# Optimization experiments

Measured on AMD Instinct MI355X. Metric: run time of the kernel, lower is better.

The kernel has to match this reference:

```python
import jax, jax.numpy as jnp
import numpy as np

K = 1024          # num_embeddings
D = 256           # embedding_dim
COMMIT = 0.25
DECAY = 0.99
EPS = 1e-05


def setup_inputs() -> dict:
    key = jax.random.key(0)
    k1, k2 = jax.random.split(key)
    inputs = jax.random.normal(k1, (16, 4096, D), dtype=jnp.float32)
    weight = jax.random.normal(k2, (K, D), dtype=jnp.float32) * 0.1
    ema_cluster_size = jnp.zeros((K,), dtype=jnp.float32)
    ema_embedding_avg = weight  # initialized as a clone of the weights
    return {
        "inputs": inputs,
        "weight": weight,
        "ema_cluster_size": ema_cluster_size,
        "ema_embedding_avg": ema_embedding_avg,
    }


def reference(inputs, weight, ema_cluster_size, ema_embedding_avg):
    B = inputs.shape[0]
    flat = inputs.reshape(-1, D)                      # [N, D]
    dist = (
        jnp.sum(flat * flat, axis=1, keepdims=True)
        + jnp.sum(weight * weight, axis=1)
        - 2.0 * (flat @ weight.T)
    )                                                 # [N, K]
    idx = jnp.argmin(dist, axis=1)                    # [N] int
    # one-hot @ weight == gather
    quantized = weight[idx].reshape(inputs.shape)

    # --- EMA codebook update (training-mode side effects, returned as outputs) ---
    counts = jax.ops.segment_sum(jnp.ones_like(idx, dtype=jnp.float32), idx, num_segments=K)
    emb_sum = jax.ops.segment_sum(flat, idx, num_segments=K)  # one_hot.T @ flat
    new_cluster_size = DECAY * ema_cluster_size + (1.0 - DECAY) * counts
    new_embedding_avg = DECAY * ema_embedding_avg + (1.0 - DECAY) * emb_sum
    n = jnp.sum(new_cluster_size)
    cs = (new_cluster_size + EPS) / (n + K * EPS) * n
    new_weight = new_embedding_avg / cs[:, None]

    # --- losses + straight-through estimator ---
    e_latent_loss = jnp.mean((jax.lax.stop_gradient(quantized) - inputs) ** 2)
    q_latent_loss = jnp.mean((quantized - jax.lax.stop_gradient(inputs)) ** 2)
    vq_loss = q_latent_loss + COMMIT * e_latent_loss
    quantized_st = inputs + jax.lax.stop_gradient(quantized - inputs)

    return (
        quantized_st,
        vq_loss,
        idx.reshape(B, -1),
        new_weight,
        new_cluster_size,
        new_embedding_avg,
    )
```

## Files before the change

kernel.cpp:

```cpp
#include <hip/hip_runtime.h>

#define KC 1024
#define DD 256
#define NROWS 65536
#define BM 128
#define NT 512
#define RESCUE_EPS 0.02f
#define RB 8

typedef _Float16 f16x8 __attribute__((ext_vector_type(8)));
typedef __fp16 fp16x2 __attribute__((ext_vector_type(2)));
typedef float f32x4 __attribute__((ext_vector_type(4)));
typedef const __attribute__((address_space(1))) unsigned int* gptr_t;
typedef __attribute__((address_space(3))) unsigned int* lptr_t;

__global__ void wprep(const float* __restrict__ W, _Float16* __restrict__ wh,
                      float* __restrict__ se, float4* __restrict__ WT4) {
    int k = blockIdx.x, lane = threadIdx.x;
    float4 v = reinterpret_cast<const float4*>(W + (size_t)k * DD)[lane];
    union { fp16x2 h2[2]; uint2 u; } cv;
    cv.h2[0] = __builtin_amdgcn_cvt_pkrtz(v.x, v.y);
    cv.h2[1] = __builtin_amdgcn_cvt_pkrtz(v.z, v.w);
    *reinterpret_cast<uint2*>(wh + (size_t)k * DD + lane * 4) = cv.u;
    WT4[(size_t)lane * KC + k] = v;
    double s = (double)v.x * v.x + (double)v.y * v.y + (double)v.z * v.z + (double)v.w * v.w;
    for (int m = 32; m >= 1; m >>= 1) s += __shfl_xor(s, m, 64);
    if (lane == 0) se[k] = (float)s;
}

__global__ __launch_bounds__(NT, 2) void vq_mfma(
    const float* __restrict__ X,
    const _Float16* __restrict__ wh,
    const float* __restrict__ se,
    float* __restrict__ out_q, float* __restrict__ out_idx,
    int* __restrict__ idx_int, float* __restrict__ sx_out,
    int* __restrict__ flags, int* __restrict__ count,
    float* __restrict__ counts, double* __restrict__ loss_acc)
{
    __shared__ __align__(16) _Float16 wt[2][64 * 256];
    __shared__ float sxs[BM];
    __shared__ float ses[KC];
    __shared__ int argidx[BM];
    __shared__ double lred[8];

    const int tid = threadIdx.x;
    const int row0 = blockIdx.x * BM;
    const int w = tid >> 6, lane = tid & 63;
    const int m = lane & 15, g = lane >> 4;

    for (int i = tid; i < KC; i += NT) ses[i] = se[i];

    f16x8 ahr[8];
    {
        const float* xr = X + (size_t)(row0 + w * 16 + m) * DD;
        float p0 = 0.f, p1 = 0.f, p2 = 0.f, p3 = 0.f;
#pragma unroll
        for (int ks = 0; ks < 8; ++ks) {
            float4 a = *reinterpret_cast<const float4*>(xr + ks * 32 + g * 8);
            float4 b = *reinterpret_cast<const float4*>(xr + ks * 32 + g * 8 + 4);
            union { fp16x2 h2[4]; f16x8 h8; } cv;
            cv.h2[0] = __builtin_amdgcn_cvt_pkrtz(a.x, a.y);
            cv.h2[1] = __builtin_amdgcn_cvt_pkrtz(a.z, a.w);
            cv.h2[2] = __builtin_amdgcn_cvt_pkrtz(b.x, b.y);
            cv.h2[3] = __builtin_amdgcn_cvt_pkrtz(b.z, b.w);
            ahr[ks] = cv.h8;
            p0 = fmaf(a.x, a.x, fmaf(b.x, b.x, p0));
            p1 = fmaf(a.y, a.y, fmaf(b.y, b.y, p1));
            p2 = fmaf(a.z, a.z, fmaf(b.z, b.z, p2));
            p3 = fmaf(a.w, a.w, fmaf(b.w, b.w, p3));
        }
        float ss = (p0 + p1) + (p2 + p3);
        ss += __shfl_xor(ss, 16, 64);
        ss += __shfl_xor(ss, 32, 64);
        if (g == 0) sxs[w * 16 + m] = ss;
    }

    size_t srcoff[4];
    unsigned ldsoff[4];
#pragma unroll
    for (int p = 0; p < 4; ++p) {
        int gi = p * NT + tid;
        int code = gi >> 5, j = gi & 31;
        int kq = j ^ (code & 31);
        srcoff[p] = (size_t)code * DD + kq * 8;
        ldsoff[p] = gi * 8;
    }
    auto stage = [&](int ct, int buf) {
        const _Float16* b = wh + (size_t)ct * 64 * DD;
#pragma unroll
        for (int p = 0; p < 4; ++p)
            __builtin_amdgcn_global_load_lds((gptr_t)(const void*)(b + srcoff[p]),
                                             (lptr_t)(void*)&wt[buf][ldsoff[p]], 16, 0, 0);
    };

    stage(0, 0);
    __syncthreads();

    float b1[4], b2[4];
    int i1[4];
#pragma unroll
    for (int j = 0; j < 4; ++j) { b1[j] = 3.4e38f; b2[j] = 3.4e38f; i1[j] = 0; }

    float sxr[4];
#pragma unroll
    for (int j = 0; j < 4; ++j) sxr[j] = sxs[w * 16 + g * 4 + j];

    for (int ct = 0; ct < 16; ++ct) {
        const int buf = ct & 1;
        if (ct < 15) stage(ct + 1, buf ^ 1);

        const _Float16* wtb = wt[buf];
        f32x4 acc[4];
#pragma unroll
        for (int cs = 0; cs < 4; ++cs) acc[cs] = (f32x4){0.f, 0.f, 0.f, 0.f};

#pragma unroll
        for (int ks = 0; ks < 8; ++ks) {
            const int kq = ks * 4 + g;
#pragma unroll
            for (int cs = 0; cs < 4; ++cs) {
                const int code = cs * 16 + m;
                const int L = code * 32 + (kq ^ (code & 31));
                f16x8 bh = *reinterpret_cast<const f16x8*>(wtb + L * 8);
                acc[cs] = __builtin_amdgcn_mfma_f32_16x16x32_f16(ahr[ks], bh, acc[cs], 0, 0, 0);
            }
        }
#pragma unroll
        for (int cs = 0; cs < 4; ++cs) {
            const int code = ct * 64 + cs * 16 + m;
            const float sec = ses[code];
#pragma unroll
            for (int j = 0; j < 4; ++j) {
                float s = fmaf(-2.0f, acc[cs][j], sxr[j] + sec);
                if (s < b1[j]) { b2[j] = b1[j]; b1[j] = s; i1[j] = code; }
                else if (s < b2[j]) { b2[j] = s; }
            }
        }
        __syncthreads();
    }

#pragma unroll
    for (int j = 0; j < 4; ++j) {
        float v1 = b1[j], v2 = b2[j];
        int ix = i1[j];
        for (int mm = 1; mm < 16; mm <<= 1) {
            float ov1 = __shfl_xor(v1, mm, 64);
            int oi = __shfl_xor(ix, mm, 64);
            float ov2 = __shfl_xor(v2, mm, 64);
            float nv2 = fminf(fminf(v2, ov2), fmaxf(v1, ov1));
            if (ov1 < v1 || (ov1 == v1 && oi < ix)) { v1 = ov1; ix = oi; }
            v2 = nv2;
        }
        if (m == 0) {
            int rl = w * 16 + g * 4 + j;
            argidx[rl] = ix;
            if (v2 - v1 < RESCUE_EPS) {
                int p = atomicAdd(count, 1);
                flags[p] = row0 + rl;
            }
        }
    }
    __syncthreads();

    if (tid < BM) {
        int row = row0 + tid;
        int k = argidx[tid];
        idx_int[row] = k;
        out_idx[row] = (float)k;
        sx_out[row] = sxs[tid];
        atomicAdd(&counts[k], 1.0f);
    }

    {
        float lacc = 0.0f;
        const int rl = w * 16 + m;
        const int row = row0 + rl;
        const int k = argidx[rl];
        const _Float16* qh = wh + (size_t)k * DD;
        float* orow = out_q + (size_t)row * DD;
#pragma unroll
        for (int ks = 0; ks < 8; ++ks) {
            const int col = ks * 32 + g * 8;
            union { uint4 u; _Float16 h[8]; } qv, xv;
            qv.u = *reinterpret_cast<const uint4*>(qh + col);
            xv.u = *reinterpret_cast<uint4*>(&ahr[ks]);
            float o8[8];
#pragma unroll
            for (int q = 0; q < 8; ++q) {
                float qf = (float)qv.h[q];
                float df = qf - (float)xv.h[q];
                o8[q] = qf;
                lacc = fmaf(df, df, lacc);
            }
            *reinterpret_cast<float4*>(orow + col)     = *reinterpret_cast<float4*>(&o8[0]);
            *reinterpret_cast<float4*>(orow + col + 4) = *reinterpret_cast<float4*>(&o8[4]);
        }
        for (int mm = 32; mm >= 1; mm >>= 1) lacc += __shfl_xor(lacc, mm, 64);
        if (lane == 0) lred[w] = (double)lacc;
    }
    __syncthreads();
    if (tid == 0) {
        double t = 0.0;
        for (int i = 0; i < 8; ++i) t += lred[i];
        atomicAdd(loss_acc, t);
    }
}

__global__ __launch_bounds__(256) void rescue(
    const float* __restrict__ X, const float4* __restrict__ WT4,
    const float* __restrict__ Wf,
    const float* __restrict__ se, const float* __restrict__ sx,
    const int* __restrict__ flags, const int* __restrict__ count,
    int* __restrict__ idx_int, float* __restrict__ out_idx,
    float* __restrict__ out_q, float* __restrict__ counts,
    double* __restrict__ loss_acc)
{
    __shared__ __align__(16) float xs[RB][DD];
    __shared__ float rv[RB][256];
    __shared__ int ri[RB][256];
    __shared__ float sxr_s[RB];
    __shared__ int rows_s[RB];
    __shared__ int kn_s[RB], ko_s[RB];
    __shared__ double dred[4];
    const int t = threadIdx.x;
    const int n = count[0];

    for (int base = blockIdx.x * RB; base < n; base += gridDim.x * RB) {
        const int nb = min(RB, n - base);
        for (int idx = t; idx < nb * 64; idx += 256) {
            int r = idx >> 6, c4 = idx & 63;
            float4 v = reinterpret_cast<const float4*>(X + (size_t)flags[base + r] * DD)[c4];
            *reinterpret_cast<float4*>(&xs[r][c4 * 4]) = v;
        }
        if (t < nb) { rows_s[t] = flags[base + t]; sxr_s[t] = sx[flags[base + t]]; }
        __syncthreads();

        float acc[4][RB];
#pragma unroll
        for (int cc = 0; cc < 4; ++cc)
#pragma unroll
            for (int r = 0; r < RB; ++r) acc[cc][r] = 0.0f;

        float4 wv[4], wn[4];
#pragma unroll
        for (int cc = 0; cc < 4; ++cc) wv[cc] = WT4[(size_t)0 * KC + cc * 256 + t];

        for (int d4 = 0; d4 < 64; ++d4) {
            const int dn = (d4 < 63) ? d4 + 1 : 63;
#pragma unroll
            for (int cc = 0; cc < 4; ++cc) wn[cc] = WT4[(size_t)dn * KC + cc * 256 + t];
#pragma unroll
            for (int r = 0; r < RB; ++r) {
                float4 xv = *reinterpret_cast<const float4*>(&xs[r][d4 * 4]);
#pragma unroll
                for (int cc = 0; cc < 4; ++cc)
                    acc[cc][r] = fmaf(xv.w, wv[cc].w, fmaf(xv.z, wv[cc].z,
                                 fmaf(xv.y, wv[cc].y, fmaf(xv.x, wv[cc].x, acc[cc][r]))));
            }
#pragma unroll
            for (int cc = 0; cc < 4; ++cc) wv[cc] = wn[cc];
        }

        float best[RB];
        int bidx[RB];
#pragma unroll
        for (int r = 0; r < RB; ++r) { best[r] = 3.4e38f; bidx[r] = 0; }
#pragma unroll
        for (int cc = 0; cc < 4; ++cc) {
            const int c = cc * 256 + t;
            const float sec = se[c];
#pragma unroll
            for (int r = 0; r < RB; ++r) {
                float s = __fsub_rn(__fadd_rn(sxr_s[r], sec), __fmul_rn(2.0f, acc[cc][r]));
                if (s < best[r] || (s == best[r] && c < bidx[r])) { best[r] = s; bidx[r] = c; }
            }
        }
#pragma unroll
        for (int r = 0; r < RB; ++r) { rv[r][t] = best[r]; ri[r][t] = bidx[r]; }
        __syncthreads();

        for (int sft = 128; sft >= 1; sft >>= 1) {
            if (t < sft) {
#pragma unroll
                for (int r = 0; r < RB; ++r) {
                    float ov = rv[r][t + sft];
                    int oi = ri[r][t + sft];
                    if (ov < rv[r][t] || (ov == rv[r][t] && oi < ri[r][t])) {
                        rv[r][t] = ov; ri[r][t] = oi;
                    }
                }
            }
            __syncthreads();
        }
        if (t < nb) {
            int row = rows_s[t];
            int kn = ri[t][0], ko = idx_int[row];
            kn_s[t] = kn; ko_s[t] = ko;
            if (kn != ko) {
                idx_int[row] = kn;
                out_idx[row] = (float)kn;
                atomicAdd(&counts[ko], -1.0f);
                atomicAdd(&counts[kn], 1.0f);
            }
        }
        __syncthreads();

        for (int r = 0; r < nb; ++r) {
            const int ko = ko_s[r], kn = kn_s[r];
            if (kn != ko) {
                const int row = rows_s[r];
                float x = xs[r][t];
                float qo = Wf[(size_t)ko * DD + t];
                float qn = Wf[(size_t)kn * DD + t];
                float dfn = qn - x, dfo = qo - x;
                out_q[(size_t)row * DD + t] = x + dfn;
                double dl = (double)dfn * dfn - (double)dfo * dfo;
                for (int mm = 32; mm >= 1; mm >>= 1) dl += __shfl_xor(dl, mm, 64);
                if ((t & 63) == 0) dred[t >> 6] = dl;
                __syncthreads();
                if (t == 0) atomicAdd(loss_acc, dred[0] + dred[1] + dred[2] + dred[3]);
                __syncthreads();
            }
        }
        __syncthreads();
    }
}

__global__ void finprefix(const float* __restrict__ ema_cs, float* __restrict__ ncs_buf,
                          const double* __restrict__ loss_acc, float* __restrict__ out_loss,
                          float* __restrict__ n_out, int* __restrict__ off,
                          int* __restrict__ cur)
{
    __shared__ float red[1024];
    __shared__ int s[1024];
    int t = threadIdx.x;
    const float OM = (float)(1.0 - 0.99);
    float cnt = ncs_buf[t];
    s[t] = (int)cnt;
    float ncs = __fadd_rn(__fmul_rn(0.99f, ema_cs[t]), __fmul_rn(OM, cnt));
    ncs_buf[t] = ncs;
    red[t] = ncs;
    __syncthreads();
    for (int st = 512; st >= 1; st >>= 1) {
        if (t < st) red[t] += red[t + st];
        __syncthreads();
    }
    if (t == 0) {
        n_out[0] = red[0];
        float el = (float)(loss_acc[0] / 16777216.0);
        out_loss[0] = __fadd_rn(el, __fmul_rn(0.25f, el));
    }
    for (int d = 1; d < 1024; d <<= 1) {
        int v = (t >= d) ? s[t - d] : 0;
        __syncthreads();
        s[t] += v;
        __syncthreads();
    }
    off[t] = (t == 0) ? 0 : s[t - 1];
    cur[t] = 0;
    if (t == 0) off[1024] = NROWS;
}

__global__ __launch_bounds__(256) void scatter_rows(
    const int* __restrict__ idx_int, const int* __restrict__ off,
    int* __restrict__ cur, int* __restrict__ sorted) {
    int i = blockIdx.x * 256 + threadIdx.x;
    int k = idx_int[i];
    int p = atomicAdd(&cur[k], 1);
    sorted[off[k] + p] = i;
}

__global__ __launch_bounds__(256) void embfin2(
    const float* __restrict__ X, const int* __restrict__ off,
    const int* __restrict__ sorted, const float* __restrict__ ema_avg,
    const float* __restrict__ ncs, const float* __restrict__ n_ptr,
    float* __restrict__ out_avg, float* __restrict__ out_w)
{
    const int k = blockIdx.x, t = threadIdx.x;
    const int s0 = off[k], s1 = off[k + 1];
    float a0 = 0.f, a1 = 0.f, a2 = 0.f, a3 = 0.f;
    int i = s0;
    for (; i + 4 <= s1; i += 4) {
        int r0 = sorted[i], r1 = sorted[i + 1], r2 = sorted[i + 2], r3 = sorted[i + 3];
        a0 += X[(size_t)r0 * DD + t];
        a1 += X[(size_t)r1 * DD + t];
        a2 += X[(size_t)r2 * DD + t];
        a3 += X[(size_t)r3 * DD + t];
    }
    for (; i < s1; ++i) a0 += X[(size_t)sorted[i] * DD + t];
    float total = (a0 + a1) + (a2 + a3);

    const float OM = (float)(1.0 - 0.99);
    const float KEPS = (float)(1024.0 * 1e-5);
    size_t o = (size_t)k * DD + t;
    float avg = __fadd_rn(__fmul_rn(0.99f, ema_avg[o]), __fmul_rn(OM, total));
    float n = n_ptr[0];
    float cs = __fmul_rn(__fdiv_rn(__fadd_rn(ncs[k], 1e-5f), __fadd_rn(n, KEPS)), n);
    out_avg[o] = avg;
    out_w[o] = __fdiv_rn(avg, cs);
}

extern "C" void kernel_launch(void* const* d_in, const int* in_sizes, int n_in,
                              void* d_out, int out_size, void* d_ws, size_t ws_size,
                              hipStream_t stream) {
    const float* X = (const float*)d_in[0];
    const float* W = (const float*)d_in[1];
    const float* ema_cs = (const float*)d_in[2];
    const float* ema_avg = (const float*)d_in[3];

    float* out = (float*)d_out;
    float* out_q    = out;
    float* out_loss = out + 16777216;
    float* out_idx  = out + 16777217;
    float* out_w    = out + 16842753;
    float* out_ncs  = out + 17104897;
    float* out_avg  = out + 17105921;

    char* ws = (char*)d_ws;
    float* se      = (float*)(ws + 0);
    float* n_ptr   = (float*)(ws + 4096);
    double* loss   = (double*)(ws + 4112);
    int*   count   = (int*)(ws + 4128);
    _Float16* wh   = (_Float16*)(ws + 8192);
    float* sx      = (float*)(ws + 1056768);
    int*   idx_int = (int*)(ws + 1318912);
    int*   flags   = (int*)(ws + 1581056);
    float4* WT4    = (float4*)(ws + 2097152);
    int*   off     = (int*)(ws + 3145728);
    int*   cur     = (int*)(ws + 3153920);
    int*   sorted  = (int*)(ws + 3158016);

    hipMemsetAsync(out_ncs, 0, 1024 * sizeof(float), stream);
    hipMemsetAsync(loss, 0, sizeof(double), stream);
    hipMemsetAsync(count, 0, sizeof(int), stream);

    wprep<<<KC, 64, 0, stream>>>(W, wh, se, WT4);
    vq_mfma<<<NROWS / BM, NT, 0, stream>>>(X, wh, se, out_q, out_idx,
                                           idx_int, sx, flags, count,
                                           out_ncs, loss);
    rescue<<<512, 256, 0, stream>>>(X, WT4, W, se, sx, flags, count, idx_int, out_idx,
                                    out_q, out_ncs, loss);
    finprefix<<<1, 1024, 0, stream>>>(ema_cs, out_ncs, loss, out_loss, n_ptr, off, cur);
    scatter_rows<<<NROWS / 256, 256, 0, stream>>>(idx_int, off, cur, sorted);
    embfin2<<<KC, 256, 0, stream>>>(X, off, sorted, ema_avg, out_ncs, n_ptr,
                                    out_avg, out_w);
}
```

Measured before the change: 183.7 us.

## Give each wave two row tiles so codebook fragments are reused; fold memsets into wprep

The MFMA distance kernel now runs 256 threads per block, and each wave computes two 16-row tiles against every codebook fragment it reads from LDS. This halves the LDS reads per MFMA and raises the register footprint per thread. Staging now issues 8 global-to-LDS loads per thread to keep filling the same 64-code tile. The three hipMemsetAsync calls are removed and the zeroing of counts, loss and flag counter is done inside wprep, saving launch overhead.

New measurement: 175.8 us. 1.04x faster.

```diff
diff --git a/kernel.cpp b/kernel.cpp
--- a/kernel.cpp
+++ b/kernel.cpp
@@ -4,7 +4,7 @@
 #define DD 256
 #define NROWS 65536
 #define BM 128
-#define NT 512
+#define NT 256
 #define RESCUE_EPS 0.02f
 #define RB 8
 
@@ -15,7 +15,9 @@
 typedef __attribute__((address_space(3))) unsigned int* lptr_t;
 
 __global__ void wprep(const float* __restrict__ W, _Float16* __restrict__ wh,
-                      float* __restrict__ se, float4* __restrict__ WT4) {
+                      float* __restrict__ se, float4* __restrict__ WT4,
+                      float* __restrict__ counts, double* __restrict__ loss,
+                      int* __restrict__ flagcnt) {
     int k = blockIdx.x, lane = threadIdx.x;
     float4 v = reinterpret_cast<const float4*>(W + (size_t)k * DD)[lane];
     union { fp16x2 h2[2]; uint2 u; } cv;
@@ -25,7 +27,11 @@
     WT4[(size_t)lane * KC + k] = v;
     double s = (double)v.x * v.x + (double)v.y * v.y + (double)v.z * v.z + (double)v.w * v.w;
     for (int m = 32; m >= 1; m >>= 1) s += __shfl_xor(s, m, 64);
-    if (lane == 0) se[k] = (float)s;
+    if (lane == 0) {
+        se[k] = (float)s;
+        counts[k] = 0.0f;
+        if (k == 0) { loss[0] = 0.0; flagcnt[0] = 0; }
+    }
 }
 
 __global__ __launch_bounds__(NT, 2) void vq_mfma(
@@ -41,7 +47,7 @@
     __shared__ float sxs[BM];
     __shared__ float ses[KC];
     __shared__ int argidx[BM];
-    __shared__ double lred[8];
+    __shared__ double lred[4];
 
     const int tid = threadIdx.x;
     const int row0 = blockIdx.x * BM;
@@ -50,9 +56,10 @@
 
     for (int i = tid; i < KC; i += NT) ses[i] = se[i];
 
-    f16x8 ahr[8];
-    {
-        const float* xr = X + (size_t)(row0 + w * 16 + m) * DD;
+    f16x8 ahr[2][8];
+#pragma unroll
+    for (int rt = 0; rt < 2; ++rt) {
+        const float* xr = X + (size_t)(row0 + w * 32 + rt * 16 + m) * DD;
         float p0 = 0.f, p1 = 0.f, p2 = 0.f, p3 = 0.f;
 #pragma unroll
         for (int ks = 0; ks < 8; ++ks) {
@@ -63,7 +70,7 @@
             cv.h2[1] = __builtin_amdgcn_cvt_pkrtz(a.z, a.w);
             cv.h2[2] = __builtin_amdgcn_cvt_pkrtz(b.x, b.y);
             cv.h2[3] = __builtin_amdgcn_cvt_pkrtz(b.z, b.w);
-            ahr[ks] = cv.h8;
+            ahr[rt][ks] = cv.h8;
             p0 = fmaf(a.x, a.x, fmaf(b.x, b.x, p0));
             p1 = fmaf(a.y, a.y, fmaf(b.y, b.y, p1));
             p2 = fmaf(a.z, a.z, fmaf(b.z, b.z, p2));
@@ -72,23 +79,22 @@
         float ss = (p0 + p1) + (p2 + p3);
         ss += __shfl_xor(ss, 16, 64);
         ss += __shfl_xor(ss, 32, 64);
-        if (g == 0) sxs[w * 16 + m] = ss;
-    }
-
-    size_t srcoff[4];
-    unsigned ldsoff[4];
-#pragma unroll
-    for (int p = 0; p < 4; ++p) {
+        if (g == 0) sxs[w * 32 + rt * 16 + m] = ss;
+    }
+
+    unsigned srcoff[8], ldsoff[8];
+#pragma unroll
+    for (int p = 0; p < 8; ++p) {
         int gi = p * NT + tid;
         int code = gi >> 5, j = gi & 31;
         int kq = j ^ (code & 31);
-        srcoff[p] = (size_t)code * DD + kq * 8;
+        srcoff[p] = (unsigned)(code * DD + kq * 8);
         ldsoff[p] = gi * 8;
     }
     auto stage = [&](int ct, int buf) {
         const _Float16* b = wh + (size_t)ct * 64 * DD;
 #pragma unroll
-        for (int p = 0; p < 4; ++p)
+        for (int p = 0; p < 8; ++p)
             __builtin_amdgcn_global_load_lds((gptr_t)(const void*)(b + srcoff[p]),
                                              (lptr_t)(void*)&wt[buf][ldsoff[p]], 16, 0, 0);
     };
@@ -96,23 +102,30 @@
     stage(0, 0);
     __syncthreads();
 
-    float b1[4], b2[4];
-    int i1[4];
-#pragma unroll
-    for (int j = 0; j < 4; ++j) { b1[j] = 3.4e38f; b2[j] = 3.4e38f; i1[j] = 0; }
-
-    float sxr[4];
-#pragma unroll
-    for (int j = 0; j < 4; ++j) sxr[j] = sxs[w * 16 + g * 4 + j];
+    float b1[2][4], b2[2][4];
+    int i1[2][4];
+#pragma unroll
+    for (int rt = 0; rt < 2; ++rt)
+#pragma unroll
+        for (int j = 0; j < 4; ++j) { b1[rt][j] = 3.4e38f; b2[rt][j] = 3.4e38f; i1[rt][j] = 0; }
+
+    float sxr[2][4];
+#pragma unroll
+    for (int rt = 0; rt < 2; ++rt)
+#pragma unroll
+        for (int j = 0; j < 4; ++j) sxr[rt][j] = sxs[w * 32 + rt * 16 + g * 4 + j];
 
     for (int ct = 0; ct < 16; ++ct) {
         const int buf = ct & 1;
         if (ct < 15) stage(ct + 1, buf ^ 1);
 
         const _Float16* wtb = wt[buf];
-        f32x4 acc[4];
-#pragma unroll
-        for (int cs = 0; cs < 4; ++cs) acc[cs] = (f32x4){0.f, 0.f, 0.f, 0.f};
+        f32x4 acc0[4], acc1[4];
+#pragma unroll
+        for (int cs = 0; cs < 4; ++cs) {
+            acc0[cs] = (f32x4){0.f, 0.f, 0.f, 0.f};
+            acc1[cs] = (f32x4){0.f, 0.f, 0.f, 0.f};
+        }
 
 #pragma unroll
         for (int ks = 0; ks < 8; ++ks) {
@@ -122,7 +135,8 @@
                 const int code = cs * 16 + m;
                 const int L = code * 32 + (kq ^ (code & 31));
                 f16x8 bh = *reinterpret_cast<const f16x8*>(wtb + L * 8);
-                acc[cs] = __builtin_amdgcn_mfma_f32_16x16x32_f16(ahr[ks], bh, acc[cs], 0, 0, 0);
+                acc0[cs] = __builtin_amdgcn_mfma_f32_16x16x32_f16(ahr[0][ks], bh, acc0[cs], 0, 0, 0);
+                acc1[cs] = __builtin_amdgcn_mfma_f32_16x16x32_f16(ahr[1][ks], bh, acc1[cs], 0, 0, 0);
             }
         }
 #pragma unroll
@@ -130,36 +144,42 @@
             const int code = ct * 64 + cs * 16 + m;
             const float sec = ses[code];
 #pragma unroll
-            for (int j = 0; j < 4; ++j) {
-                float s = fmaf(-2.0f, acc[cs][j], sxr[j] + sec);
-                if (s < b1[j]) { b2[j] = b1[j]; b1[j] = s; i1[j] = code; }
-                else if (s < b2[j]) { b2[j] = s; }
-            }
-        }
-        __syncthreads();
-    }
-
-#pragma unroll
-    for (int j = 0; j < 4; ++j) {
-        float v1 = b1[j], v2 = b2[j];
-        int ix = i1[j];
-        for (int mm = 1; mm < 16; mm <<= 1) {
-            float ov1 = __shfl_xor(v1, mm, 64);
-            int oi = __shfl_xor(ix, mm, 64);
-            float ov2 = __shfl_xor(v2, mm, 64);
-            float nv2 = fminf(fminf(v2, ov2), fmaxf(v1, ov1));
-            if (ov1 < v1 || (ov1 == v1 && oi < ix)) { v1 = ov1; ix = oi; }
-            v2 = nv2;
-        }
-        if (m == 0) {
-            int rl = w * 16 + g * 4 + j;
-            argidx[rl] = ix;
-            if (v2 - v1 < RESCUE_EPS) {
-                int p = atomicAdd(count, 1);
-                flags[p] = row0 + rl;
-            }
-        }
-    }
+            for (int rt = 0; rt < 2; ++rt) {
+                f32x4 A = rt ? acc1[cs] : acc0[cs];
+#pragma unroll
+                for (int j = 0; j < 4; ++j) {
+                    float s = fmaf(-2.0f, A[j], sxr[rt][j] + sec);
+                    if (s < b1[rt][j]) { b2[rt][j] = b1[rt][j]; b1[rt][j] = s; i1[rt][j] = code; }
+                    else if (s < b2[rt][j]) { b2[rt][j] = s; }
+                }
+            }
+        }
+        __syncthreads();
+    }
+
+#pragma unroll
+    for (int rt = 0; rt < 2; ++rt)
+#pragma unroll
+        for (int j = 0; j < 4; ++j) {
+            float v1 = b1[rt][j], v2 = b2[rt][j];
+            int ix = i1[rt][j];
+            for (int mm = 1; mm < 16; mm <<= 1) {
+                float ov1 = __shfl_xor(v1, mm, 64);
+                int oi = __shfl_xor(ix, mm, 64);
+                float ov2 = __shfl_xor(v2, mm, 64);
+                float nv2 = fminf(fminf(v2, ov2), fmaxf(v1, ov1));
+                if (ov1 < v1 || (ov1 == v1 && oi < ix)) { v1 = ov1; ix = oi; }
+                v2 = nv2;
+            }
+            if (m == 0) {
+                int rl = w * 32 + rt * 16 + g * 4 + j;
+                argidx[rl] = ix;
+                if (v2 - v1 < RESCUE_EPS) {
+                    int p = atomicAdd(count, 1);
+                    flags[p] = row0 + rl;
+                }
+            }
+        }
     __syncthreads();
 
     if (tid < BM) {
@@ -173,35 +193,37 @@
 
     {
         float lacc = 0.0f;
-        const int rl = w * 16 + m;
-        const int row = row0 + rl;
-        const int k = argidx[rl];
-        const _Float16* qh = wh + (size_t)k * DD;
-        float* orow = out_q + (size_t)row * DD;
-#pragma unroll
-        for (int ks = 0; ks < 8; ++ks) {
-            const int col = ks * 32 + g * 8;
-            union { uint4 u; _Float16 h[8]; } qv, xv;
-            qv.u = *reinterpret_cast<const uint4*>(qh + col);
-            xv.u = *reinterpret_cast<uint4*>(&ahr[ks]);
-            float o8[8];
-#pragma unroll
-            for (int q = 0; q < 8; ++q) {
-                float qf = (float)qv.h[q];
-                float df = qf - (float)xv.h[q];
-                o8[q] = qf;
-                lacc = fmaf(df, df, lacc);
-            }
-            *reinterpret_cast<float4*>(orow + col)     = *reinterpret_cast<float4*>(&o8[0]);
-            *reinterpret_cast<float4*>(orow + col + 4) = *reinterpret_cast<float4*>(&o8[4]);
+#pragma unroll
+        for (int rt = 0; rt < 2; ++rt) {
+            const int rl = w * 32 + rt * 16 + m;
+            const int row = row0 + rl;
+            const int k = argidx[rl];
+            const _Float16* qh = wh + (size_t)k * DD;
+            float* orow = out_q + (size_t)row * DD;
+#pragma unroll
+            for (int ks = 0; ks < 8; ++ks) {
+                const int col = ks * 32 + g * 8;
+                union { uint4 u; _Float16 h[8]; } qv, xv;
+                qv.u = *reinterpret_cast<const uint4*>(qh + col);
+                xv.u = *reinterpret_cast<uint4*>(&ahr[rt][ks]);
+                float o8[8];
+#pragma unroll
+                for (int q = 0; q < 8; ++q) {
+                    float qf = (float)qv.h[q];
+                    float df = qf - (float)xv.h[q];
+                    o8[q] = qf;
+                    lacc = fmaf(df, df, lacc);
+                }
+                *reinterpret_cast<float4*>(orow + col)     = *reinterpret_cast<float4*>(&o8[0]);
+                *reinterpret_cast<float4*>(orow + col + 4) = *reinterpret_cast<float4*>(&o8[4]);
+            }
         }
         for (int mm = 32; mm >= 1; mm >>= 1) lacc += __shfl_xor(lacc, mm, 64);
         if (lane == 0) lred[w] = (double)lacc;
     }
     __syncthreads();
     if (tid == 0) {
-        double t = 0.0;
-        for (int i = 0; i < 8; ++i) t += lred[i];
+        double t = lred[0] + lred[1] + lred[2] + lred[3];
         atomicAdd(loss_acc, t);
     }
 }
@@ -430,11 +452,7 @@
     int*   cur     = (int*)(ws + 3153920);
     int*   sorted  = (int*)(ws + 3158016);
 
-    hipMemsetAsync(out_ncs, 0, 1024 * sizeof(float), stream);
-    hipMemsetAsync(loss, 0, sizeof(double), stream);
-    hipMemsetAsync(count, 0, sizeof(int), stream);
-
-    wprep<<<KC, 64, 0, stream>>>(W, wh, se, WT4);
+    wprep<<<KC, 64, 0, stream>>>(W, wh, se, WT4, out_ncs, loss, count);
     vq_mfma<<<NROWS / BM, NT, 0, stream>>>(X, wh, se, out_q, out_idx,
                                            idx_int, sx, flags, count,
                                            out_ncs, loss);
```
